# Optimization experiments

Hardware: AMD Instinct MI355X
Metric: run time of the kernel (lower is better)

The kernel has to match this reference:

```python
import jax, jax.numpy as jnp
import numpy as np

B, H, W, D = 8, 64, 64, 1024


def setup_inputs() -> dict:
    key = jax.random.key(0)
    ks = jax.random.split(key, 10)
    s = 0.02
    return {
        "x": jax.random.normal(ks[0], (B, H, W, D), dtype=jnp.float32),
        "Wq": jax.random.normal(ks[1], (D, D), dtype=jnp.float32) * s,
        "bq": jnp.zeros((D,), dtype=jnp.float32),
        "Wk": jax.random.normal(ks[2], (D, D), dtype=jnp.float32) * s,
        "bk": jnp.zeros((D,), dtype=jnp.float32),
        "Wv": jax.random.normal(ks[3], (D, D), dtype=jnp.float32) * s,
        "bv": jnp.zeros((D,), dtype=jnp.float32),
        "Wo": jax.random.normal(ks[4], (D, D), dtype=jnp.float32) * s,
        "bo": jnp.zeros((D,), dtype=jnp.float32),
        "sigma": jnp.ones((1,), dtype=jnp.float32),
    }


def _dist(n, dtype):
    i = jnp.arange(n)
    return jnp.square(i[:, None] - i[None, :]).astype(dtype)


def reference(x, Wq, bq, Wk, bk, Wv, bv, Wo, bo, sigma):
    b, h, w, d = x.shape
    gw = 1.0 / (2.0 * jnp.square(sigma))  # scalar (shape [1])
    q = jnp.einsum('bhwd,ed->bhwe', x, Wq) + bq
    k = jnp.einsum('bhwd,ed->bhwe', x, Wk) + bk
    v = jnp.einsum('bhwd,ed->bhwe', x, Wv) + bv
    # row attention: attend across width within each row
    r_qk = jnp.einsum('bhwd,bhkd->bhwk', q, k) - gw[0] * _dist(w, x.dtype)
    r_attn = jax.nn.softmax(r_qk, axis=-1)               # [b,h,w,w]
    r_out = jnp.einsum('bhwk,bhkd->bhwd', r_attn, v)
    # column attention: attend across height within each column
    c_qk = jnp.einsum('bhwd,bgwd->bwhg', q, k) - gw[0] * _dist(h, x.dtype)
    c_attn = jax.nn.softmax(c_qk, axis=-1)               # [b,w,h,h]
    c_out = jnp.einsum('bwhg,bgwd->bhwd', c_attn, v)
    out = r_out + c_out
    return jnp.einsum('bhwd,ed->bhwe', out, Wo) + bo
```

## Files before the change

### kernel.cpp

```cpp
#include <hip/hip_runtime.h>


typedef _Float16 f16;
typedef __attribute__((ext_vector_type(8))) _Float16 f16x8;
typedef __attribute__((ext_vector_type(4))) float f32x4;

__global__ __launch_bounds__(256) void k_cvt_all(
    const float* __restrict__ x, const float* __restrict__ Wq,
    const float* __restrict__ Wk, const float* __restrict__ Wv,
    const float* __restrict__ Wo, f16* __restrict__ xb,
    f16* __restrict__ wqkv, f16* __restrict__ wob) {
  const int stride = gridDim.x * blockDim.x;
  const int X8 = 33554432 / 8;
  const int W8 = 1048576 / 8;
  const int total = X8 + 4 * W8;
  for (int i = blockIdx.x * blockDim.x + threadIdx.x; i < total; i += stride) {
    const float* src; f16* dst; int o8;
    if (i < X8) { src = x; dst = xb; o8 = i; }
    else {
      int j = i - X8; int seg = j >> 17; o8 = j & (W8 - 1);
      if (seg == 0)      { src = Wq; dst = wqkv; }
      else if (seg == 1) { src = Wk; dst = wqkv + 1048576; }
      else if (seg == 2) { src = Wv; dst = wqkv + 2097152; }
      else               { src = Wo; dst = wob; }
    }
    const float4* p = (const float4*)src + (size_t)o8 * 2;
    float4 a = p[0]; float4 b = p[1];
    f16x8 o;
    o[0]=(f16)a.x; o[1]=(f16)a.y; o[2]=(f16)a.z; o[3]=(f16)a.w;
    o[4]=(f16)b.x; o[5]=(f16)b.y; o[6]=(f16)b.z; o[7]=(f16)b.w;
    *(f16x8*)(dst + (size_t)o8 * 8) = o;
  }
}

template<bool C_F32>
__global__ __launch_bounds__(512, 2) void k_gemm256(const f16* __restrict__ A,
                                                    const f16* __restrict__ B,
                                                    const float* __restrict__ b0,
                                                    const float* __restrict__ b1,
                                                    const float* __restrict__ b2,
                                                    void* __restrict__ Cout,
                                                    int M, int N, int K) {
  __shared__ f16 smem[2][2][2][128 * 64];

  const int tid = threadIdx.x;
  const int lane = tid & 63;
  const int wid = tid >> 6;
  const int wr = wid >> 2;
  const int wc = wid & 3;
  const int lane_r = lane & 15;
  const int g = lane >> 4;

  const int nwg = gridDim.x;
  const int bid = blockIdx.x;
  const int swz = (bid & 7) * (nwg >> 3) + (bid >> 3);
  const int nbn = N >> 8;
  const int bm = swz / nbn, bn = swz % nbn;

  const int u0 = ((g) ^ (lane_r & 7)) * 8;
  const int u1 = ((4 + g) ^ (lane_r & 7)) * 8;
  const int arow = lane >> 3;
  const int acol = ((lane & 7) ^ (lane >> 3)) * 8;

  const f16* Ag[2] = { A + (size_t)(bm * 256) * K, A + (size_t)(bm * 256 + 128) * K };
  const f16* Bg[2] = { B + (size_t)(bn * 256) * K, B + (size_t)(bn * 256 + 128) * K };

  f32x4 acc[8][4];
#pragma unroll
  for (int i = 0; i < 8; ++i)
#pragma unroll
    for (int j = 0; j < 4; ++j) acc[i][j] = (f32x4){0.f, 0.f, 0.f, 0.f};

#define STAGE(gbase, kt, lbase)                                                     \
  {                                                                                 \
    _Pragma("unroll") for (int i_ = 0; i_ < 2; ++i_) {                              \
      const f16* g_ = (gbase) + (size_t)(wid * 16 + i_ * 8 + arow) * K + (kt) * 64 + acol; \
      __builtin_amdgcn_global_load_lds(                                             \
          (const __attribute__((address_space(1))) void*)g_,                        \
          (__attribute__((address_space(3))) void*)((lbase) + (wid * 16 + i_ * 8) * 64), \
          16, 0, 0);                                                                \
    }                                                                               \
  }

#define MFMAQ(q)                                                                    \
  _Pragma("unroll") for (int mm = 0; mm < 2; ++mm)                                  \
  _Pragma("unroll") for (int n = 0; n < 4; ++n) {                                   \
    acc[(q)*2 + mm][n] = __builtin_amdgcn_mfma_f32_16x16x32_f16(afrag[mm][0], bfrag[n][0], acc[(q)*2 + mm][n], 0, 0, 0); \
    acc[(q)*2 + mm][n] = __builtin_amdgcn_mfma_f32_16x16x32_f16(afrag[mm][1], bfrag[n][1], acc[(q)*2 + mm][n], 0, 0, 0); \
  }

#define READ_A(q)                                                                   \
  _Pragma("unroll") for (int mm = 0; mm < 2; ++mm) {                                \
    const int rb_ = ((q)*32 + mm * 16 + lane_r) * 64;                               \
    afrag[mm][0] = *(const f16x8*)&As_[rb_ + u0];                                   \
    afrag[mm][1] = *(const f16x8*)&As_[rb_ + u1];                                   \
  }

#define KTILE(t, slot, vm, st)                                                      \
  {                                                                                 \
    f16* As_ = smem[slot][0][wr];                                                   \
    f16* Bs_ = smem[slot][1][wc >> 1];                                              \
    f16x8 bfrag[4][2], afrag[2][2];                                                 \
    asm volatile("s_waitcnt vmcnt(%0)" :: "n"(vm) : "memory");                      \
    __builtin_amdgcn_s_barrier();                                                   \
    _Pragma("unroll") for (int n = 0; n < 4; ++n) {                                 \
      const int rb_ = ((wc & 1) * 64 + n * 16 + lane_r) * 64;                       \
      bfrag[n][0] = *(const f16x8*)&Bs_[rb_ + u0];                                  \
      bfrag[n][1] = *(const f16x8*)&Bs_[rb_ + u1];                                  \
    }                                                                               \
    READ_A(0)                                                                       \
    asm volatile("s_waitcnt lgkmcnt(4)" ::: "memory");                              \
    __builtin_amdgcn_s_barrier();                                                   \
    if ((st) >= 1) {                                                                \
      STAGE(Ag[0], (t) + 1, smem[(slot) ^ 1][0][0]);                                \
      STAGE(Ag[1], (t) + 1, smem[(slot) ^ 1][0][1]);                                \
    }                                                                               \
    if ((st) == 2) {                                                                \
      STAGE(Bg[0], (t) + 2, smem[slot][1][0]);                                      \
      STAGE(Bg[1], (t) + 2, smem[slot][1][1]);                                      \
    }                                                                               \
    __builtin_amdgcn_s_setprio(1);                                                  \
    MFMAQ(0)                                                                        \
    READ_A(1)                                                                       \
    MFMAQ(1)                                                                        \
    READ_A(2)                                                                       \
    MFMAQ(2)                                                                        \
    READ_A(3)                                                                       \
    MFMAQ(3)                                                                        \
    __builtin_amdgcn_s_setprio(0);                                                  \
  }

  const int nt = K >> 6;

  STAGE(Ag[0], 0, smem[0][0][0]);
  STAGE(Ag[1], 0, smem[0][0][1]);
  STAGE(Bg[0], 0, smem[0][1][0]);
  STAGE(Bg[1], 0, smem[0][1][1]);
  STAGE(Bg[0], 1, smem[1][1][0]);
  STAGE(Bg[1], 1, smem[1][1][1]);

  for (int t = 0; t + 3 < nt; t += 2) {
    KTILE(t, 0, 4, 2)
    KTILE(t + 1, 1, 4, 2)
  }
  KTILE(nt - 2, 0, 4, 1)
  KTILE(nt - 1, 1, 0, 0)

  const int mrow0 = bm * 256 + wr * 128 + (lane >> 4) * 4;
  const int ncol0 = bn * 256 + wc * 64 + (lane & 15);
#pragma unroll
  for (int n = 0; n < 4; ++n) {
    const int col = ncol0 + n * 16;
    const float* bp = (col < 1024) ? b0 : ((col < 2048) ? b1 : b2);
    const float bvv = bp[col & 1023];
#pragma unroll
    for (int mrep = 0; mrep < 8; ++mrep) {
#pragma unroll
      for (int r = 0; r < 4; ++r) {
        const int row = mrow0 + mrep * 16 + r;
        const float val = acc[mrep][n][r] + bvv;
        if (C_F32) ((float*)Cout)[(size_t)row * N + col] = val;
        else       ((f16*)Cout)[(size_t)row * N + col] = (f16)val;
      }
    }
  }
#undef KTILE
#undef READ_A
#undef MFMAQ
#undef STAGE
}

template<bool IS_COL>
__global__ __launch_bounds__(256) void k_attn(const f16* __restrict__ qkv,
                                              f16* __restrict__ attn,
                                              const float* __restrict__ sigma) {
  __shared__ union { float S[64][68]; f16 Vt[256][72]; } sm;
  __shared__ f16 P[64][72];

  const int tid = threadIdx.x;
  const int lane = tid & 63;
  const int wid = tid >> 6;
  const int blk = blockIdx.x;

  size_t tok0; int tstr;
  if (IS_COL) { tok0 = (size_t)(blk >> 6) * 4096 + (blk & 63); tstr = 64; }
  else        { tok0 = (size_t)blk * 64;                       tstr = 1;  }
  const size_t ibase = tok0 * 3072;  const int istr = tstr * 3072;
  const size_t obase = tok0 * 1024;  const int ostr = tstr * 1024;

  const float sg = sigma[0];
  const float gw = 0.5f / (sg * sg);

  const int m0 = wid * 16;
  const int lr = lane & 15;
  const int lq = lane >> 4;

  f32x4 sacc[4];
#pragma unroll
  for (int nt = 0; nt < 4; ++nt) sacc[nt] = (f32x4){0.f, 0.f, 0.f, 0.f};
  const f16* qp = qkv + ibase + (size_t)(m0 + lr) * istr + lq * 8;
  const f16* kp = qkv + ibase + 1024 + (size_t)lr * istr + lq * 8;
#pragma unroll 2
  for (int ks = 0; ks < 32; ++ks) {
    f16x8 af = *(const f16x8*)(qp + ks * 32);
#pragma unroll
    for (int nt = 0; nt < 4; ++nt) {
      f16x8 bfr = *(const f16x8*)(kp + (size_t)nt * 16 * istr + ks * 32);
      sacc[nt] = __builtin_amdgcn_mfma_f32_16x16x32_f16(af, bfr, sacc[nt], 0, 0, 0);
    }
  }
#pragma unroll
  for (int nt = 0; nt < 4; ++nt)
#pragma unroll
    for (int r = 0; r < 4; ++r) {
      const int row = m0 + lq * 4 + r;
      const int col = nt * 16 + lr;
      const float dd = (float)(row - col);
      sm.S[row][col] = sacc[nt][r] - gw * dd * dd;
    }
  __syncthreads();

  {
    const int r = tid >> 2, s4 = tid & 3;
    const float4* sp = (const float4*)&sm.S[r][s4 * 16];
    float vals[16];
#pragma unroll
    for (int j = 0; j < 4; ++j) {
      float4 t = sp[j];
      vals[j * 4 + 0] = t.x; vals[j * 4 + 1] = t.y; vals[j * 4 + 2] = t.z; vals[j * 4 + 3] = t.w;
    }
    float mx = vals[0];
#pragma unroll
    for (int j = 1; j < 16; ++j) mx = fmaxf(mx, vals[j]);
    mx = fmaxf(mx, __shfl_xor(mx, 1));
    mx = fmaxf(mx, __shfl_xor(mx, 2));
    float sum = 0.f;
#pragma unroll
    for (int j = 0; j < 16; ++j) { vals[j] = __expf(vals[j] - mx); sum += vals[j]; }
    sum += __shfl_xor(sum, 1);
    sum += __shfl_xor(sum, 2);
    const float inv = 1.f / sum;
#pragma unroll
    for (int j = 0; j < 16; ++j) P[r][s4 * 16 + j] = (f16)(vals[j] * inv);
  }
  __syncthreads();

  const f16x8 af0 = *(const f16x8*)&P[m0 + lr][lq * 8];
  const f16x8 af1 = *(const f16x8*)&P[m0 + lr][32 + lq * 8];

  const int kr = tid & 63;
  const int cg = tid >> 6;
  const f16* vp = qkv + ibase + 2048 + (size_t)kr * istr;

  for (int c = 0; c < 4; ++c) {
#pragma unroll
    for (int j8 = 0; j8 < 8; ++j8) {
      const int cl = cg * 64 + j8 * 8;
      f16x8 vv = *(const f16x8*)(vp + c * 256 + cl);
#pragma unroll
      for (int e = 0; e < 8; ++e) sm.Vt[cl + e][kr] = vv[e];
    }
    __syncthreads();
#pragma unroll
    for (int nt = 0; nt < 16; ++nt) {
      const f16x8 bf0 = *(const f16x8*)&sm.Vt[nt * 16 + lr][lq * 8];
      const f16x8 bf1 = *(const f16x8*)&sm.Vt[nt * 16 + lr][32 + lq * 8];
      f32x4 o = (f32x4){0.f, 0.f, 0.f, 0.f};
      o = __builtin_amdgcn_mfma_f32_16x16x32_f16(af0, bf0, o, 0, 0, 0);
      o = __builtin_amdgcn_mfma_f32_16x16x32_f16(af1, bf1, o, 0, 0, 0);
#pragma unroll
      for (int r = 0; r < 4; ++r) {
        const int row = m0 + lq * 4 + r;
        const int col = c * 256 + nt * 16 + lr;
        const size_t addr = obase + (size_t)row * ostr + col;
        float val = o[r];
        if (IS_COL) val += (float)attn[addr];
        attn[addr] = (f16)val;
      }
    }
    __syncthreads();
  }
}

extern "C" void kernel_launch(void* const* d_in, const int* in_sizes, int n_in,
                              void* d_out, int out_size, void* d_ws, size_t ws_size,
                              hipStream_t stream) {
  const float* x  = (const float*)d_in[0];
  const float* Wq = (const float*)d_in[1];
  const float* bq = (const float*)d_in[2];
  const float* Wk = (const float*)d_in[3];
  const float* bk = (const float*)d_in[4];
  const float* Wv = (const float*)d_in[5];
  const float* bv = (const float*)d_in[6];
  const float* Wo = (const float*)d_in[7];
  const float* bo = (const float*)d_in[8];
  const float* sg = (const float*)d_in[9];

  const int M = 8 * 64 * 64;
  const size_t NE = (size_t)M * 1024;

  f16* xb   = (f16*)d_ws;
  f16* wqkv = xb + NE;
  f16* wob  = wqkv + 3 * 1024 * 1024;
  f16* qkv  = wob + 1024 * 1024;

  k_cvt_all<<<2048, 256, 0, stream>>>(x, Wq, Wk, Wv, Wo, xb, wqkv, wob);

  k_gemm256<false><<<(M / 256) * (3072 / 256), 512, 0, stream>>>(
      xb, wqkv, bq, bk, bv, qkv, M, 3072, 1024);

  f16* attn = xb;
  k_attn<false><<<512, 256, 0, stream>>>(qkv, attn, sg);
  k_attn<true><<<512, 256, 0, stream>>>(qkv, attn, sg);

  k_gemm256<true><<<(M / 256) * (1024 / 256), 512, 0, stream>>>(
      attn, wob, bo, bo, bo, (float*)d_out, M, 1024, 1024);
}
```

Measured before the change: 512.6 us.

## Prefetch V chunks into registers and stage attention output through LDS for vector stores

The V chunk for the next column block is now loaded into registers while MFMAs run on the current chunk, and the first chunk is prefetched before the QK phase so global latency overlaps compute. The output tile is written to a shared-memory buffer first and then stored to global memory as 16-byte vectors, including a vectorized read-modify-write for the column pass. This replaces scattered 2-byte stores with coalesced ones. In exchange it raises register pressure (64 extra f16 per thread) and LDS use, which may lower occupancy.

```diff
diff --git a/kernel.cpp b/kernel.cpp
--- a/kernel.cpp
+++ b/kernel.cpp
@@ -174,7 +174,10 @@
 __global__ __launch_bounds__(256) void k_attn(const f16* __restrict__ qkv,
                                               f16* __restrict__ attn,
                                               const float* __restrict__ sigma) {
-  __shared__ union { float S[64][68]; f16 Vt[256][72]; } sm;
+  __shared__ union {
+    float S[64][68];
+    struct { f16 Vt[256][72]; f16 O[64][264]; } pv;
+  } sm;
   __shared__ f16 P[64][72];
 
   const int tid = threadIdx.x;
@@ -194,6 +197,14 @@
   const int m0 = wid * 16;
   const int lr = lane & 15;
   const int lq = lane >> 4;
+
+  const int kr = tid & 63;
+  const int cg = tid >> 6;
+  const f16* vp = qkv + ibase + 2048 + (size_t)kr * istr;
+  f16x8 vreg[8];
+#pragma unroll
+  for (int j8 = 0; j8 < 8; ++j8)
+    vreg[j8] = *(const f16x8*)(vp + cg * 64 + j8 * 8);
 
   f32x4 sacc[4];
 #pragma unroll
@@ -248,34 +259,53 @@
   const f16x8 af0 = *(const f16x8*)&P[m0 + lr][lq * 8];
   const f16x8 af1 = *(const f16x8*)&P[m0 + lr][32 + lq * 8];
 
-  const int kr = tid & 63;
-  const int cg = tid >> 6;
-  const f16* vp = qkv + ibase + 2048 + (size_t)kr * istr;
+#pragma unroll
+  for (int j8 = 0; j8 < 8; ++j8) {
+    const int cl = cg * 64 + j8 * 8;
+#pragma unroll
+    for (int e = 0; e < 8; ++e) sm.pv.Vt[cl + e][kr] = vreg[j8][e];
+  }
+  __syncthreads();
 
   for (int c = 0; c < 4; ++c) {
-#pragma unroll
-    for (int j8 = 0; j8 < 8; ++j8) {
-      const int cl = cg * 64 + j8 * 8;
-      f16x8 vv = *(const f16x8*)(vp + c * 256 + cl);
-#pragma unroll
-      for (int e = 0; e < 8; ++e) sm.Vt[cl + e][kr] = vv[e];
-    }
-    __syncthreads();
+    if (c < 3) {
+#pragma unroll
+      for (int j8 = 0; j8 < 8; ++j8)
+        vreg[j8] = *(const f16x8*)(vp + (c + 1) * 256 + cg * 64 + j8 * 8);
+    }
 #pragma unroll
     for (int nt = 0; nt < 16; ++nt) {
-      const f16x8 bf0 = *(const f16x8*)&sm.Vt[nt * 16 + lr][lq * 8];
-      const f16x8 bf1 = *(const f16x8*)&sm.Vt[nt * 16 + lr][32 + lq * 8];
+      const f16x8 bf0 = *(const f16x8*)&sm.pv.Vt[nt * 16 + lr][lq * 8];
+      const f16x8 bf1 = *(const f16x8*)&sm.pv.Vt[nt * 16 + lr][32 + lq * 8];
       f32x4 o = (f32x4){0.f, 0.f, 0.f, 0.f};
       o = __builtin_amdgcn_mfma_f32_16x16x32_f16(af0, bf0, o, 0, 0, 0);
       o = __builtin_amdgcn_mfma_f32_16x16x32_f16(af1, bf1, o, 0, 0, 0);
 #pragma unroll
-      for (int r = 0; r < 4; ++r) {
-        const int row = m0 + lq * 4 + r;
-        const int col = c * 256 + nt * 16 + lr;
-        const size_t addr = obase + (size_t)row * ostr + col;
-        float val = o[r];
-        if (IS_COL) val += (float)attn[addr];
-        attn[addr] = (f16)val;
+      for (int r = 0; r < 4; ++r)
+        sm.pv.O[m0 + lq * 4 + r][nt * 16 + lr] = (f16)o[r];
+    }
+    __syncthreads();
+
+    {
+      const int orow = tid >> 2, cs = tid & 3;
+      const size_t gaddr = obase + (size_t)orow * ostr + c * 256 + cs * 64;
+#pragma unroll
+      for (int j = 0; j < 8; ++j) {
+        f16x8 ov = *(const f16x8*)&sm.pv.O[orow][cs * 64 + j * 8];
+        if (IS_COL) {
+          f16x8 old = *(const f16x8*)(attn + gaddr + j * 8);
+#pragma unroll
+          for (int e = 0; e < 8; ++e) ov[e] = (f16)((float)ov[e] + (float)old[e]);
+        }
+        *(f16x8*)(attn + gaddr + j * 8) = ov;
+      }
+    }
+    if (c < 3) {
+#pragma unroll
+      for (int j8 = 0; j8 < 8; ++j8) {
+        const int cl = cg * 64 + j8 * 8;
+#pragma unroll
+        for (int e = 0; e < 8; ++e) sm.pv.Vt[cl + e][kr] = vreg[j8][e];
       }
     }
     __syncthreads();
```

New measurement: 501.6 us (median of 2 runs). 1.02x faster.
